# Kernel tuning notes

Hardware: AMD Instinct MI355X
Metric: run time of the kernel (lower is better)

## Reference

```python
import jax, jax.numpy as jnp
import numpy as np


def setup_inputs() -> dict:
    key = jax.random.key(0)
    kE, kD, kW, kU, kV = jax.random.split(key, 5)
    B, T, H, U = 32, 2048, 1024, 1024
    scale = 0.02
    return {
        "enc_out": jax.random.normal(kE, (B, T, H), dtype=jnp.float32),
        "dec_hidden": jax.random.normal(kD, (B, H), dtype=jnp.float32),
        "Wa": jax.random.normal(kW, (H, U), dtype=jnp.float32) * scale,
        "Ua": jax.random.normal(kU, (H, U), dtype=jnp.float32) * scale,
        "Va": jax.random.normal(kV, (U,), dtype=jnp.float32) * scale,
    }


def reference(enc_out, dec_hidden, Wa, Ua, Va):
    # Bahdanau additive attention.
    # enc_out: [B, T, H]; dec_hidden: [B, H]; Wa: [H, U]; Ua: [H, U]; Va: [U]
    dec_proj = jnp.einsum("bh,hu->bu", dec_hidden, Wa)          # [B, U]
    enc_proj = jnp.einsum("bth,hu->btu", enc_out, Ua)            # [B, T, U]
    s = jnp.tanh(enc_proj + dec_proj[:, None, :])                # [B, T, U]
    score = jnp.einsum("btu,u->bt", s, Va)                       # [B, T]
    alpha = jax.nn.softmax(score, axis=-1)                       # [B, T]
    context = jnp.einsum("bt,bth->bh", alpha, enc_out)           # [B, H]
    return context
```

## Files before the change

kernel.cpp:

```cpp
#include <hip/hip_runtime.h>
#include <stdint.h>


#define B_ 32
#define T_ 2048
#define H_ 1024
#define U_ 1024
#define M_ (B_ * T_)

typedef __bf16 bf16x8 __attribute__((ext_vector_type(8)));
typedef float f32x4 __attribute__((ext_vector_type(4)));

__device__ __forceinline__ unsigned f2b(float f) {
  unsigned u = __float_as_uint(f);
  return (u + 0x7FFFu + ((u >> 16) & 1u)) >> 16;
}
__device__ __forceinline__ float b2f(unsigned short u) {
  return __uint_as_float(((unsigned)u) << 16);
}
__device__ __forceinline__ float fast_tanh(float x) {
  float xc = fminf(fmaxf(x, -12.f), 12.f);
  float t = exp2f(xc * 2.885390081777927f);
  return (t - 1.f) * __builtin_amdgcn_rcpf(t + 1.f);
}

#define AS1 __attribute__((address_space(1)))
#define AS3 __attribute__((address_space(3)))
__device__ __forceinline__ void gld_lds16(const void* g, void* l) {
  __builtin_amdgcn_global_load_lds((AS1 const void*)g, (AS3 void*)l, 16, 0, 0);
}

__device__ __forceinline__ void BAR() {
  __builtin_amdgcn_sched_barrier(0);
  __builtin_amdgcn_s_barrier();
  __builtin_amdgcn_sched_barrier(0);
}

__global__ __launch_bounds__(256) void prep_k(
    const float4* __restrict__ enc, uint4* __restrict__ outA,
    const float* __restrict__ Ua, uint4* __restrict__ Ub,
    const float* __restrict__ dh, const float* __restrict__ Wa,
    float* __restrict__ dp4, float* __restrict__ outz) {
  const int bx = blockIdx.x;
  const int tx = threadIdx.x;

  if (bx < 4096) {
    __shared__ uint4 L4[128 * 17];
    const int band = bx;
    const int mt = band >> 3;
    const int R = (band & 7) << 4;
    const float4* src = enc + (size_t)band * 4096;
#pragma unroll
    for (int i = 0; i < 8; ++i) {
      int p = i * 256 + tx;
      int r = p >> 7, pc = p & 127;
      float4 a = src[r * 256 + pc * 2];
      float4 b = src[r * 256 + pc * 2 + 1];
      uint4 o;
      o.x = f2b(a.x) | (f2b(a.y) << 16);
      o.y = f2b(a.z) | (f2b(a.w) << 16);
      o.z = f2b(b.x) | (f2b(b.y) << 16);
      o.w = f2b(b.z) | (f2b(b.w) << 16);
      L4[pc * 17 + r] = o;
    }
    __syncthreads();
    const int r2 = tx & 15, kq = (tx >> 4) & 3, w = tx >> 6;
#pragma unroll
    for (int j = 0; j < 8; ++j) {
      int k8 = j * 16 + w * 4 + kq;
      outA[((size_t)mt * 128 + k8) * 128 + R + r2] = L4[k8 * 17 + r2];
    }
  } else if (bx < 4608) {
    int id = (bx - 4096) * 256 + tx;
    int h8 = id >> 10, u = id & 1023;
    const float* p = Ua + (size_t)(h8 << 3) * U_ + u;
    uint4 o;
    o.x = f2b(p[0]) | (f2b(p[U_]) << 16);
    o.y = f2b(p[2 * U_]) | (f2b(p[3 * U_]) << 16);
    o.z = f2b(p[4 * U_]) | (f2b(p[5 * U_]) << 16);
    o.w = f2b(p[6 * U_]) | (f2b(p[7 * U_]) << 16);
    Ub[(size_t)h8 * U_ + u] = o;
  } else if (bx < 5120) {
    int g = bx - 4608;
    const int u = (g & 3) * 256 + tx;
    const int b = (g >> 2) & 31, hz = g >> 7;
    const float* d = dh + b * H_ + hz * 256;
    const float* w = Wa + (size_t)(hz * 256) * U_ + u;
    float a0 = 0.f, a1 = 0.f, a2 = 0.f, a3 = 0.f;
#pragma unroll 4
    for (int h = 0; h < 256; h += 4) {
      a0 = fmaf(d[h + 0], w[(size_t)(h + 0) * U_], a0);
      a1 = fmaf(d[h + 1], w[(size_t)(h + 1) * U_], a1);
      a2 = fmaf(d[h + 2], w[(size_t)(h + 2) * U_], a2);
      a3 = fmaf(d[h + 3], w[(size_t)(h + 3) * U_], a3);
    }
    dp4[((hz * B_ + b) * U_) + u] = (a0 + a1) + (a2 + a3);
  } else {
    outz[(bx - 5120) * 256 + tx] = 0.f;
  }
}

__global__ __launch_bounds__(256, 2) void score_gemm_k(
    const unsigned short* __restrict__ encA,
    const unsigned short* __restrict__ Ub,
    const float* __restrict__ dp4,
    const float* __restrict__ Va,
    float* __restrict__ score8)
{
  __shared__ union {
    struct {
      alignas(16) unsigned short As[2][8][128][8];
      alignas(16) unsigned short Bs[2][8][128][8];
    } t;
    float sred[128 * 33];
  } sm;

  const int bx = blockIdx.x;
  const int mtile = ((bx >> 6) << 3) | (bx & 7), ntile = (bx >> 3) & 7;
  const int m0 = mtile << 7, n0 = ntile << 7;
  const int tid = threadIdx.x;
  const int wv = tid >> 6, ln = tid & 63;
  const int wm = wv & 1, wn = wv >> 1;
  const int quad = ln >> 4, l16 = ln & 15;

  f32x4 acc[4][4];
  const f32x4 zero = {0.f, 0.f, 0.f, 0.f};
#pragma unroll
  for (int i = 0; i < 4; ++i)
#pragma unroll
    for (int j = 0; j < 4; ++j) acc[i][j] = zero;

  const unsigned short* encT = encA + (size_t)mtile * (128 * 128 * 8);

  auto STAGE = [&](int kt, int bsel) {
    const int kb = kt << 3;
#pragma unroll
    for (int c = 0; c < 4; ++c) {
      int chunk = (wv << 2) + c;
      int k8 = chunk >> 1, half = (chunk & 1) << 6;
      const unsigned short* ga =
          encT + (((size_t)(kb + k8) * 128) + half + ln) * 8;
      gld_lds16(ga, &sm.t.As[bsel][k8][half][0]);
      const unsigned short* gb =
          Ub + (((size_t)(kb + k8) * U_) + n0 + half + ln) * 8;
      gld_lds16(gb, &sm.t.Bs[bsel][k8][half][0]);
    }
  };

  STAGE(0, 0);

  for (int kt = 0; kt < 16; ++kt) {
    const int cb = kt & 1, nb = cb ^ 1;
    if (kt < 15) {
      STAGE(kt + 1, nb);
      asm volatile("s_waitcnt vmcnt(8)" ::: "memory");
    } else {
      asm volatile("s_waitcnt vmcnt(0)" ::: "memory");
    }
    BAR();

#pragma unroll
    for (int kk = 0; kk < 2; ++kk) {
      int k8b = (kk << 2) + quad;
      bf16x8 af[4], bf[4];
#pragma unroll
      for (int mt = 0; mt < 4; ++mt)
        af[mt] =
            *(const bf16x8*)&sm.t.As[cb][k8b][(wm << 6) + (mt << 4) + l16][0];
#pragma unroll
      for (int nt = 0; nt < 4; ++nt)
        bf[nt] =
            *(const bf16x8*)&sm.t.Bs[cb][k8b][(wn << 6) + (nt << 4) + l16][0];
#pragma unroll
      for (int mt = 0; mt < 4; ++mt)
#pragma unroll
        for (int nt = 0; nt < 4; ++nt)
          acc[mt][nt] = __builtin_amdgcn_mfma_f32_16x16x32_bf16(
              af[mt], bf[nt], acc[mt][nt], 0, 0, 0);
    }
    BAR();
  }

  const int bq = m0 >> 11;
  float va[4], dpv[4];
#pragma unroll
  for (int nt = 0; nt < 4; ++nt) {
    int col = n0 + (wn << 6) + (nt << 4) + l16;
    va[nt] = Va[col];
    dpv[nt] = dp4[bq * U_ + col] + dp4[B_ * U_ + bq * U_ + col] +
              dp4[2 * B_ * U_ + bq * U_ + col] + dp4[3 * B_ * U_ + bq * U_ + col];
  }
  __syncthreads();
#pragma unroll
  for (int mt = 0; mt < 4; ++mt) {
#pragma unroll
    for (int r = 0; r < 4; ++r) {
      float v = 0.f;
#pragma unroll
      for (int nt = 0; nt < 4; ++nt)
        v += fast_tanh(acc[mt][nt][r] + dpv[nt]) * va[nt];
      int row = (wm << 6) + (mt << 4) + (quad << 2) + r;
      sm.sred[row * 33 + (wn << 4) + l16] = v;
    }
  }
  __syncthreads();
  if (tid < 128) {
    const float* p = &sm.sred[tid * 33];
    float s = 0.f;
#pragma unroll
    for (int j = 0; j < 32; ++j) s += p[j];
    score8[(size_t)ntile * M_ + m0 + tid] = s;
  }
}

__global__ __launch_bounds__(256) void ctx_k(const uint4* __restrict__ encA,
                                             const float* __restrict__ score8,
                                             float* __restrict__ out) {
  const int b = blockIdx.y, bt = blockIdx.x, tid = threadIdx.x;
  __shared__ float s_sc[2048];
  __shared__ float a_s[128];
  __shared__ float red[4];
  __shared__ float cred[2][128][8];

  float4 v0 = {0.f, 0.f, 0.f, 0.f}, v1 = {0.f, 0.f, 0.f, 0.f};
#pragma unroll
  for (int k = 0; k < 8; ++k) {
    const float4* p = (const float4*)(score8 + (size_t)k * M_ + b * T_);
    float4 x0 = p[tid * 2], x1 = p[tid * 2 + 1];
    v0.x += x0.x; v0.y += x0.y; v0.z += x0.z; v0.w += x0.w;
    v1.x += x1.x; v1.y += x1.y; v1.z += x1.z; v1.w += x1.w;
  }
  ((float4*)s_sc)[tid * 2] = v0;
  ((float4*)s_sc)[tid * 2 + 1] = v1;

  float m = fmaxf(fmaxf(fmaxf(v0.x, v0.y), fmaxf(v0.z, v0.w)),
                  fmaxf(fmaxf(v1.x, v1.y), fmaxf(v1.z, v1.w)));
#pragma unroll
  for (int off = 32; off >= 1; off >>= 1) m = fmaxf(m, __shfl_xor(m, off));
  if ((tid & 63) == 0) red[tid >> 6] = m;
  __syncthreads();
  m = fmaxf(fmaxf(red[0], red[1]), fmaxf(red[2], red[3]));
  __syncthreads();

  const float l2e = 1.4426950408889634f;
  float sum = exp2f((v0.x - m) * l2e) + exp2f((v0.y - m) * l2e) +
              exp2f((v0.z - m) * l2e) + exp2f((v0.w - m) * l2e) +
              exp2f((v1.x - m) * l2e) + exp2f((v1.y - m) * l2e) +
              exp2f((v1.z - m) * l2e) + exp2f((v1.w - m) * l2e);
#pragma unroll
  for (int off = 32; off >= 1; off >>= 1) sum += __shfl_xor(sum, off);
  if ((tid & 63) == 0) red[tid >> 6] = sum;
  __syncthreads();
  const float inv = 1.f / (red[0] + red[1] + red[2] + red[3]);

  if (tid < 128) a_s[tid] = exp2f((s_sc[bt * 128 + tid] - m) * l2e) * inv;
  __syncthreads();

  const int tx = tid & 127, th = tid >> 7;
  const int mt = b * 16 + bt;
  const uint4* base = encA + ((size_t)mt * 128 + tx) * 128 + th * 64;
  float a[8];
#pragma unroll
  for (int j = 0; j < 8; ++j) a[j] = 0.f;
#pragma unroll 4
  for (int i = 0; i < 64; ++i) {
    float w = a_s[th * 64 + i];
    uint4 e = base[i];
    a[0] = fmaf(w, b2f((unsigned short)e.x), a[0]);
    a[1] = fmaf(w, b2f((unsigned short)(e.x >> 16)), a[1]);
    a[2] = fmaf(w, b2f((unsigned short)e.y), a[2]);
    a[3] = fmaf(w, b2f((unsigned short)(e.y >> 16)), a[3]);
    a[4] = fmaf(w, b2f((unsigned short)e.z), a[4]);
    a[5] = fmaf(w, b2f((unsigned short)(e.z >> 16)), a[5]);
    a[6] = fmaf(w, b2f((unsigned short)e.w), a[6]);
    a[7] = fmaf(w, b2f((unsigned short)(e.w >> 16)), a[7]);
  }
#pragma unroll
  for (int j = 0; j < 8; ++j) cred[th][tx][j] = a[j];
  __syncthreads();
  if (th == 0) {
    float* o = out + (size_t)b * H_ + tx * 8;
#pragma unroll
    for (int j = 0; j < 8; ++j)
      atomicAdd(&o[j], cred[0][tx][j] + cred[1][tx][j]);
  }
}

extern "C" void kernel_launch(void* const* d_in, const int* in_sizes, int n_in,
                              void* d_out, int out_size, void* d_ws, size_t ws_size,
                              hipStream_t stream) {
  const float* enc = (const float*)d_in[0];
  const float* dh  = (const float*)d_in[1];
  const float* Wa  = (const float*)d_in[2];
  const float* Ua  = (const float*)d_in[3];
  const float* Va  = (const float*)d_in[4];

  char* ws = (char*)d_ws;
  unsigned short* encA = (unsigned short*)ws;
  unsigned short* Ub   = (unsigned short*)(ws + 134217728);
  float* dp4    = (float*)(ws + 136314880);
  float* score8 = (float*)(ws + 136839168);

  prep_k<<<5248, 256, 0, stream>>>((const float4*)enc, (uint4*)encA, Ua,
                                   (uint4*)Ub, dh, Wa, dp4, (float*)d_out);
  score_gemm_k<<<4096, 256, 0, stream>>>(encA, Ub, dp4, Va, score8);
  ctx_k<<<dim3(16, 32), 256, 0, stream>>>((const uint4*)encA, score8,
                                          (float*)d_out);
}
```

Baseline: 569.3 us.

## Enlarge score GEMM tile to 256x256 with 512 threads and deeper pipelined staging

The score GEMM moves from 128x128 tiles with 256 threads to 256x256 tiles with 512 threads (8 waves, each computing 128x64). The K loop is split into quarter-stages with a 3-deep prefetch, fine-grained vmcnt waits, setprio around the MFMAs, and an XCD-aware block mapping. The tanh/Va reduction now uses lane shuffles, and the partial-score buffer shrinks from 8 slices to 4. The goal is more operand reuse per LDS byte and better overlap of global loads with compute. In exchange the per-thread accumulator count doubles and the synchronization pattern becomes more complex.

```diff
diff --git a/kernel.cpp b/kernel.cpp
--- a/kernel.cpp
+++ b/kernel.cpp
@@ -100,121 +100,153 @@
   }
 }
 
-__global__ __launch_bounds__(256, 2) void score_gemm_k(
+__global__ __launch_bounds__(512, 2) void score_gemm_k(
     const unsigned short* __restrict__ encA,
     const unsigned short* __restrict__ Ub,
     const float* __restrict__ dp4,
     const float* __restrict__ Va,
-    float* __restrict__ score8)
+    float* __restrict__ score4)
 {
   __shared__ union {
     struct {
-      alignas(16) unsigned short As[2][8][128][8];
-      alignas(16) unsigned short Bs[2][8][128][8];
+      alignas(16) unsigned short As[2][2][4][256][8];
+      alignas(16) unsigned short Bs[2][2][4][256][8];
     } t;
-    float sred[128 * 33];
+    float sred[256][4];
   } sm;
 
   const int bx = blockIdx.x;
-  const int mtile = ((bx >> 6) << 3) | (bx & 7), ntile = (bx >> 3) & 7;
-  const int m0 = mtile << 7, n0 = ntile << 7;
+  const int xcd = bx & 7, g = bx >> 3;
+  const int mt2 = xcd * 32 + (g >> 2), nt2 = g & 3;
+  const int n0 = nt2 << 8;
   const int tid = threadIdx.x;
   const int wv = tid >> 6, ln = tid & 63;
-  const int wm = wv & 1, wn = wv >> 1;
+  const int wm = wv >> 2, wn = wv & 3;
   const int quad = ln >> 4, l16 = ln & 15;
 
-  f32x4 acc[4][4];
+  auto STAGE = [&](int t, int u) {
+    const int par = t & 1;
+    const int kk = u >> 1;
+    const int k8base = t * 8 + kk * 4;
+    if (!(u & 1)) {
+#pragma unroll
+      for (int r = 0; r < 2; ++r) {
+        int i = r * 512 + tid;
+        int k8l = i >> 8, row = i & 255;
+        const unsigned short* ga =
+            encA + (((size_t)(mt2 * 2 + (row >> 7)) * 128 + k8base + k8l) * 128 +
+                    (row & 127)) * 8;
+        gld_lds16(ga, &sm.t.As[par][kk][k8l][row][0]);
+      }
+    } else {
+#pragma unroll
+      for (int r = 0; r < 2; ++r) {
+        int i = r * 512 + tid;
+        int k8l = i >> 8, col = i & 255;
+        const unsigned short* gb =
+            Ub + ((size_t)(k8base + k8l) * U_ + n0 + col) * 8;
+        gld_lds16(gb, &sm.t.Bs[par][kk][k8l][col][0]);
+      }
+    }
+  };
+
+  f32x4 acc[8][4];
   const f32x4 zero = {0.f, 0.f, 0.f, 0.f};
 #pragma unroll
-  for (int i = 0; i < 4; ++i)
+  for (int i = 0; i < 8; ++i)
 #pragma unroll
     for (int j = 0; j < 4; ++j) acc[i][j] = zero;
 
-  const unsigned short* encT = encA + (size_t)mtile * (128 * 128 * 8);
-
-  auto STAGE = [&](int kt, int bsel) {
-    const int kb = kt << 3;
-#pragma unroll
-    for (int c = 0; c < 4; ++c) {
-      int chunk = (wv << 2) + c;
-      int k8 = chunk >> 1, half = (chunk & 1) << 6;
-      const unsigned short* ga =
-          encT + (((size_t)(kb + k8) * 128) + half + ln) * 8;
-      gld_lds16(ga, &sm.t.As[bsel][k8][half][0]);
-      const unsigned short* gb =
-          Ub + (((size_t)(kb + k8) * U_) + n0 + half + ln) * 8;
-      gld_lds16(gb, &sm.t.Bs[bsel][k8][half][0]);
-    }
-  };
-
-  STAGE(0, 0);
-
+#pragma unroll
+  for (int n = 0; n < 6; ++n) STAGE(n >> 2, n & 3);
+  __builtin_amdgcn_sched_barrier(0);
+  asm volatile("s_waitcnt vmcnt(8)" ::: "memory");
+  __builtin_amdgcn_s_barrier();
+  __builtin_amdgcn_sched_barrier(0);
+
+  bf16x8 bfr[4];
+
+#pragma unroll 2
   for (int kt = 0; kt < 16; ++kt) {
-    const int cb = kt & 1, nb = cb ^ 1;
-    if (kt < 15) {
-      STAGE(kt + 1, nb);
-      asm volatile("s_waitcnt vmcnt(8)" ::: "memory");
-    } else {
-      asm volatile("s_waitcnt vmcnt(0)" ::: "memory");
-    }
-    BAR();
-
-#pragma unroll
-    for (int kk = 0; kk < 2; ++kk) {
-      int k8b = (kk << 2) + quad;
-      bf16x8 af[4], bf[4];
-#pragma unroll
-      for (int mt = 0; mt < 4; ++mt)
-        af[mt] =
-            *(const bf16x8*)&sm.t.As[cb][k8b][(wm << 6) + (mt << 4) + l16][0];
-#pragma unroll
-      for (int nt = 0; nt < 4; ++nt)
-        bf[nt] =
-            *(const bf16x8*)&sm.t.Bs[cb][k8b][(wn << 6) + (nt << 4) + l16][0];
-#pragma unroll
-      for (int mt = 0; mt < 4; ++mt)
-#pragma unroll
-        for (int nt = 0; nt < 4; ++nt)
-          acc[mt][nt] = __builtin_amdgcn_mfma_f32_16x16x32_bf16(
-              af[mt], bf[nt], acc[mt][nt], 0, 0, 0);
-    }
-    BAR();
-  }
-
-  const int bq = m0 >> 11;
+    const int par = kt & 1;
+#pragma unroll
+    for (int q = 0; q < 4; ++q) {
+      const int kk = q >> 1, mh = q & 1;
+      if (mh == 0) {
+#pragma unroll
+        for (int fn = 0; fn < 4; ++fn)
+          bfr[fn] = *(const bf16x8*)&sm.t
+                         .Bs[par][kk][quad][wn * 64 + fn * 16 + l16][0];
+      }
+      bf16x8 af[4];
+#pragma unroll
+      for (int fm = 0; fm < 4; ++fm)
+        af[fm] = *(const bf16x8*)&sm.t
+                      .As[par][kk][quad][wm * 128 + mh * 64 + fm * 16 + l16][0];
+      {
+        const int n = kt * 4 + q + 6;
+        if (n < 64) STAGE(n >> 2, n & 3);
+      }
+      __builtin_amdgcn_sched_barrier(0);
+      if (q == 1) {
+        if (kt < 15)
+          asm volatile("s_waitcnt vmcnt(8)" ::: "memory");
+        else
+          asm volatile("s_waitcnt vmcnt(0)" ::: "memory");
+      } else if (q == 3) {
+        if (kt < 14)
+          asm volatile("s_waitcnt vmcnt(8)" ::: "memory");
+        else if (kt == 14)
+          asm volatile("s_waitcnt vmcnt(4)" ::: "memory");
+      }
+      __builtin_amdgcn_s_barrier();
+      __builtin_amdgcn_sched_barrier(0);
+      __builtin_amdgcn_s_setprio(1);
+#pragma unroll
+      for (int fm = 0; fm < 4; ++fm)
+#pragma unroll
+        for (int fn = 0; fn < 4; ++fn)
+          acc[mh * 4 + fm][fn] = __builtin_amdgcn_mfma_f32_16x16x32_bf16(
+              af[fm], bfr[fn], acc[mh * 4 + fm][fn], 0, 0, 0);
+      __builtin_amdgcn_s_setprio(0);
+      BAR();
+    }
+  }
+
+  const int bq = mt2 >> 3;
   float va[4], dpv[4];
 #pragma unroll
-  for (int nt = 0; nt < 4; ++nt) {
-    int col = n0 + (wn << 6) + (nt << 4) + l16;
-    va[nt] = Va[col];
-    dpv[nt] = dp4[bq * U_ + col] + dp4[B_ * U_ + bq * U_ + col] +
-              dp4[2 * B_ * U_ + bq * U_ + col] + dp4[3 * B_ * U_ + bq * U_ + col];
-  }
-  __syncthreads();
-#pragma unroll
-  for (int mt = 0; mt < 4; ++mt) {
-#pragma unroll
-    for (int r = 0; r < 4; ++r) {
+  for (int fn = 0; fn < 4; ++fn) {
+    int col = n0 + wn * 64 + fn * 16 + l16;
+    va[fn] = Va[col];
+    dpv[fn] = dp4[bq * U_ + col] + dp4[B_ * U_ + bq * U_ + col] +
+              dp4[2 * B_ * U_ + bq * U_ + col] +
+              dp4[3 * B_ * U_ + bq * U_ + col];
+  }
+  __syncthreads();
+#pragma unroll
+  for (int i = 0; i < 8; ++i) {
+#pragma unroll
+    for (int rr = 0; rr < 4; ++rr) {
       float v = 0.f;
 #pragma unroll
-      for (int nt = 0; nt < 4; ++nt)
-        v += fast_tanh(acc[mt][nt][r] + dpv[nt]) * va[nt];
-      int row = (wm << 6) + (mt << 4) + (quad << 2) + r;
-      sm.sred[row * 33 + (wn << 4) + l16] = v;
-    }
-  }
-  __syncthreads();
-  if (tid < 128) {
-    const float* p = &sm.sred[tid * 33];
-    float s = 0.f;
-#pragma unroll
-    for (int j = 0; j < 32; ++j) s += p[j];
-    score8[(size_t)ntile * M_ + m0 + tid] = s;
+      for (int fn = 0; fn < 4; ++fn)
+        v += fast_tanh(acc[i][fn][rr] + dpv[fn]) * va[fn];
+#pragma unroll
+      for (int off = 1; off < 16; off <<= 1) v += __shfl_xor(v, off);
+      if (l16 == 0) sm.sred[wm * 128 + i * 16 + quad * 4 + rr][wn] = v;
+    }
+  }
+  __syncthreads();
+  if (tid < 256) {
+    float s = sm.sred[tid][0] + sm.sred[tid][1] + sm.sred[tid][2] +
+              sm.sred[tid][3];
+    score4[(size_t)nt2 * M_ + mt2 * 256 + tid] = s;
   }
 }
 
 __global__ __launch_bounds__(256) void ctx_k(const uint4* __restrict__ encA,
-                                             const float* __restrict__ score8,
+                                             const float* __restrict__ score4,
                                              float* __restrict__ out) {
   const int b = blockIdx.y, bt = blockIdx.x, tid = threadIdx.x;
   __shared__ float s_sc[2048];
@@ -224,8 +256,8 @@
 
   float4 v0 = {0.f, 0.f, 0.f, 0.f}, v1 = {0.f, 0.f, 0.f, 0.f};
 #pragma unroll
-  for (int k = 0; k < 8; ++k) {
-    const float4* p = (const float4*)(score8 + (size_t)k * M_ + b * T_);
+  for (int k = 0; k < 4; ++k) {
+    const float4* p = (const float4*)(score4 + (size_t)k * M_ + b * T_);
     float4 x0 = p[tid * 2], x1 = p[tid * 2 + 1];
     v0.x += x0.x; v0.y += x0.y; v0.z += x0.z; v0.w += x0.w;
     v1.x += x1.x; v1.y += x1.y; v1.z += x1.z; v1.w += x1.w;
@@ -299,11 +331,11 @@
   unsigned short* encA = (unsigned short*)ws;
   unsigned short* Ub   = (unsigned short*)(ws + 134217728);
   float* dp4    = (float*)(ws + 136314880);
-  float* score8 = (float*)(ws + 136839168);
+  float* score4 = (float*)(ws + 136839168);
 
   prep_k<<<5248, 256, 0, stream>>>((const float4*)enc, (uint4*)encA, Ua,
                                    (uint4*)Ub, dh, Wa, dp4, (float*)d_out);
-  score_gemm_k<<<4096, 256, 0, stream>>>(encA, Ub, dp4, Va, score8);
-  ctx_k<<<dim3(16, 32), 256, 0, stream>>>((const uint4*)encA, score8,
+  score_gemm_k<<<1024, 512, 0, stream>>>(encA, Ub, dp4, Va, score4);
+  ctx_k<<<dim3(16, 32), 256, 0, stream>>>((const uint4*)encA, score4,
                                           (float*)d_out);
 }
```

Result: no change. 564.9 us (-0.8%).
